# Kernel optimization log

Hardware: AMD Instinct MI355X
Metric: run time of the kernel (lower is better)

Reference implementation:

```python
import jax, jax.numpy as jnp
import numpy as np

B, S, H, NH, L, FF, V, T = 16, 256, 768, 12, 12, 3072, 30522, 9
DH = H // NH
LN_EPS = 1e-12


def _ln(x, g, b):
    m = jnp.mean(x, axis=-1, keepdims=True)
    v = jnp.mean((x - m) ** 2, axis=-1, keepdims=True)
    return (x - m) * jax.lax.rsqrt(v + LN_EPS) * g + b


def setup_inputs():
    key = jax.random.key(0)
    ks = jax.random.split(key, 20)
    n = lambda i, shape: jax.random.normal(ks[i], shape, jnp.float32) * 0.02
    lengths = jax.random.randint(ks[0], (B,), S // 2, S + 1)
    attention_mask = (jnp.arange(S)[None, :] < lengths[:, None]).astype(jnp.int32)
    return {
        "input_ids": jax.random.randint(ks[1], (B, S), 0, V),
        "attention_mask": attention_mask,
        "labels": jax.random.randint(ks[2], (B, S), 0, T),
        "word_emb": n(3, (V, H)),
        "pos_emb": n(4, (512, H)),
        "type_emb": n(5, (2, H)),
        "emb_g": jnp.ones((H,), jnp.float32), "emb_b": jnp.zeros((H,), jnp.float32),
        "lWq": n(6, (L, H, H)), "lbq": jnp.zeros((L, H), jnp.float32),
        "lWk": n(7, (L, H, H)), "lbk": jnp.zeros((L, H), jnp.float32),
        "lWv": n(8, (L, H, H)), "lbv": jnp.zeros((L, H), jnp.float32),
        "lWo": n(9, (L, H, H)), "lbo": jnp.zeros((L, H), jnp.float32),
        "lg1": jnp.ones((L, H), jnp.float32), "lb1": jnp.zeros((L, H), jnp.float32),
        "lWi": n(10, (L, H, FF)), "lbi": jnp.zeros((L, FF), jnp.float32),
        "lWf": n(11, (L, FF, H)), "lbf": jnp.zeros((L, H), jnp.float32),
        "lg2": jnp.ones((L, H), jnp.float32), "lb2": jnp.zeros((L, H), jnp.float32),
        "cls_W": n(12, (H, T)), "cls_b": jnp.zeros((T,), jnp.float32),
        "crf_start": jax.random.uniform(ks[13], (T,), jnp.float32, -0.1, 0.1),
        "crf_end": jax.random.uniform(ks[14], (T,), jnp.float32, -0.1, 0.1),
        "crf_trans": jax.random.uniform(ks[15], (T, T), jnp.float32, -0.1, 0.1),
    }


def _encoder(input_ids, attention_mask, word_emb, pos_emb, type_emb, emb_g, emb_b, layer_stack, cls_W, cls_b):
    x = word_emb[input_ids] + pos_emb[:S][None] + type_emb[0][None, None]  # [B,S,H]
    x = _ln(x, emb_g, emb_b)
    bias = (1.0 - attention_mask.astype(jnp.float32))[:, None, None, :] * -1e9  # [B,1,1,S]
    scale = 1.0 / np.sqrt(DH).astype(np.float32)

    def layer(h, p):
        Wq, bq, Wk, bk, Wv, bv, Wo, bo, g1, b1, Wi, bi, Wf, bf, g2, b2 = p
        q = (h @ Wq + bq).reshape(B, S, NH, DH)
        k = (h @ Wk + bk).reshape(B, S, NH, DH)
        v = (h @ Wv + bv).reshape(B, S, NH, DH)
        att = jax.nn.softmax(jnp.einsum('bqhd,bkhd->bhqk', q, k) * scale + bias, axis=-1)
        ctx = jnp.einsum('bhqk,bkhd->bqhd', att, v).reshape(B, S, H)
        h = _ln(h + ctx @ Wo + bo, g1, b1)
        ff = jax.nn.gelu(h @ Wi + bi, approximate=False) @ Wf + bf
        h = _ln(h + ff, g2, b2)
        return h, None

    x, _ = jax.lax.scan(layer, x, layer_stack)
    return x @ cls_W + cls_b  # [B,S,T]


def _crf_llh(em, tg, m, start, end, trans):
    # pytorch-crf forward, reduction='sum'. em [B,Lc,T], tg [B,Lc] int, m [B,Lc] bool
    mf = m.astype(em.dtype)
    em_sc = jnp.take_along_axis(em, tg[..., None], axis=-1)[..., 0]  # [B,Lc]
    tr_sc = trans[tg[:, :-1], tg[:, 1:]]                             # [B,Lc-1]
    num = start[tg[:, 0]] + em_sc[:, 0] + jnp.sum(mf[:, 1:] * (tr_sc + em_sc[:, 1:]), axis=1)
    seq_ends = jnp.sum(m.astype(jnp.int32), axis=1) - 1
    last_tag = jnp.take_along_axis(tg, seq_ends[:, None], axis=1)[:, 0]
    num = num + end[last_tag]

    def step(score, xs):
        em_t, m_t = xs
        nxt = jax.nn.logsumexp(score[:, :, None] + trans[None] + em_t[:, None, :], axis=1)
        return jnp.where(m_t[:, None], nxt, score), None

    score0 = start[None] + em[:, 0]
    score, _ = jax.lax.scan(step, score0, (em[:, 1:].transpose(1, 0, 2), m[:, 1:].transpose(1, 0)))
    den = jax.nn.logsumexp(score + end[None], axis=1)
    return jnp.sum(num - den)


def _viterbi(em, start, end, trans):
    # decode over the FULL sequence with all-ones mask (matches crf.decode(logits))
    def step(score, em_t):
        cand = score[:, :, None] + trans[None] + em_t[:, None, :]  # [B,T,T]
        return jnp.max(cand, axis=1), jnp.argmax(cand, axis=1)

    score0 = start[None] + em[:, 0]
    score, hist = jax.lax.scan(step, score0, em[:, 1:].transpose(1, 0, 2))  # hist [S-1,B,T]
    last = jnp.argmax(score + end[None], axis=1)  # [B]

    def back(tag, h):
        prev = jnp.take_along_axis(h, tag[:, None], axis=1)[:, 0]
        return prev, prev

    _, rev = jax.lax.scan(back, last, hist, reverse=True)  # rev[i] = tag at time i, i in [0,S-2]
    tags = jnp.concatenate([rev.transpose(1, 0), last[:, None]], axis=1)  # [B,S]
    return tags.astype(jnp.float32)


def reference(input_ids, attention_mask, labels, word_emb, pos_emb, type_emb, emb_g, emb_b,
              lWq, lbq, lWk, lbk, lWv, lbv, lWo, lbo, lg1, lb1, lWi, lbi, lWf, lbf, lg2, lb2,
              cls_W, cls_b, crf_start, crf_end, crf_trans):
    layer_stack = (lWq, lbq, lWk, lbk, lWv, lbv, lWo, lbo, lg1, lb1, lWi, lbi, lWf, lbf, lg2, lb2)
    logits = _encoder(input_ids, attention_mask, word_emb, pos_emb, type_emb, emb_g, emb_b, layer_stack, cls_W, cls_b)
    str_lens = jnp.sum(attention_mask, axis=-1)
    pos = jnp.arange(S)[None, :]
    mask = attention_mask.astype(bool) & (pos > 0) & (pos != (str_lens - 1)[:, None])
    tags_in = jnp.where(mask, labels, jnp.zeros_like(labels))
    loss = -_crf_llh(logits[:, 1:], tags_in[:, 1:], mask[:, 1:], crf_start, crf_end, crf_trans)
    tags = _viterbi(logits, crf_start, crf_end, crf_trans)
    return (loss, tags)
```

## Files before the change

### kernel.cpp

```cpp
#include <hip/hip_runtime.h>

#define B_ 16
#define S_ 256
#define H_ 768
#define NH_ 12
#define DH_ 64
#define L_ 12
#define FF_ 3072
#define T_ 9
#define NTOK (B_*S_)

typedef __attribute__((ext_vector_type(8))) short bfrag;
typedef __attribute__((ext_vector_type(8))) unsigned short us8;
typedef __attribute__((ext_vector_type(4))) float f4;

#define LOG2E_ 1.4426950408889634f
#define LN2_   0.6931471805599453f

__device__ inline unsigned short f2bf(float x) {
    unsigned u = __builtin_bit_cast(unsigned, x);
    return (unsigned short)((u + 0x7fffu + ((u >> 16) & 1u)) >> 16);
}
__device__ inline float bf2f(unsigned short h) {
    unsigned u = ((unsigned)h) << 16;
    return __builtin_bit_cast(float, u);
}
__device__ inline void pack8(const float* v, us8& h, us8& l) {
    #pragma unroll
    for (int j = 0; j < 8; j++) {
        unsigned short hh = f2bf(v[j]);
        h[j] = hh;
        l[j] = f2bf(v[j] - bf2f(hh));
    }
}

__global__ __launch_bounds__(256) void k_conv_w(
    const float* __restrict__ Wq, const float* __restrict__ Wk,
    const float* __restrict__ Wv, const float* __restrict__ Wo,
    const float* __restrict__ Wi, const float* __restrict__ Wf,
    const float* __restrict__ bq, const float* __restrict__ bk, const float* __restrict__ bv,
    float* __restrict__ qkvbias, unsigned short* __restrict__ Wpk)
{
    int bid = blockIdx.x;
    int tid = threadIdx.x;
    if (bid == 0) {
        for (int i = tid; i < 3 * H_; i += 256)
            qkvbias[i] = (i < H_) ? bq[i] : (i < 2 * H_) ? bk[i - H_] : bv[i - 2 * H_];
    }
    const float* src; int Kd, Nd; size_t doff; int t;
    if (bid < 576)       { int m = bid / 144; src = (m == 0) ? Wq : (m == 1) ? Wk : (m == 2) ? Wv : Wo;
                           Kd = H_; Nd = H_; doff = (size_t)m * 73728; t = bid % 144; }
    else if (bid < 1152) { src = Wi; Kd = H_; Nd = FF_; doff = 294912; t = bid - 576; }
    else                 { src = Wf; Kd = FF_; Nd = H_; doff = 589824; t = bid - 1152; }
    int ntn = Nd / 64;
    int tk = t / ntn, tn = t % ntn;
    int k0 = tk * 64, n0 = tn * 64;
    __shared__ float tile[64][65];
    int r = tid >> 6, c = tid & 63;
    #pragma unroll
    for (int i = 0; i < 16; i++)
        tile[r + i * 4][c] = src[(size_t)(k0 + r + i * 4) * Nd + n0 + c];
    __syncthreads();
    #pragma unroll
    for (int e = 0; e < 2; e++) {
        int item = tid * 2 + e;
        int nl = item >> 3, kb = item & 7;
        float v8[8];
        #pragma unroll
        for (int j = 0; j < 8; j++) v8[j] = tile[kb * 8 + j][nl];
        us8 h, l; pack8(v8, h, l);
        unsigned short* p = Wpk + (doff + (size_t)(n0 + nl) * (Kd / 8) + (k0 / 8 + kb)) * 16;
        *reinterpret_cast<us8*>(p) = h;
        *reinterpret_cast<us8*>(p + 8) = l;
    }
}

__global__ __launch_bounds__(128) void k_embed_ln(
    const int* __restrict__ ids, const float* __restrict__ wemb,
    const float* __restrict__ pemb, const float* __restrict__ temb,
    const float* __restrict__ g, const float* __restrict__ bb,
    float* __restrict__ out, unsigned short* __restrict__ out_pk)
{
    int tok = blockIdx.x;
    int s = tok & (S_ - 1);
    int id = ids[tok];
    int tid = threadIdx.x;
    bool act = tid < 96;
    int idx = tid * 8;
    float v8[8];
    float sum = 0.f;
    if (act) {
        const float4* w4 = reinterpret_cast<const float4*>(wemb + (size_t)id * H_ + idx);
        const float4* p4 = reinterpret_cast<const float4*>(pemb + (size_t)s * H_ + idx);
        const float4* t4 = reinterpret_cast<const float4*>(temb + idx);
        #pragma unroll
        for (int q = 0; q < 2; q++) {
            float4 a = w4[q], b = p4[q], c = t4[q];
            v8[q*4+0] = a.x + b.x + c.x; v8[q*4+1] = a.y + b.y + c.y;
            v8[q*4+2] = a.z + b.z + c.z; v8[q*4+3] = a.w + b.w + c.w;
        }
        #pragma unroll
        for (int j = 0; j < 8; j++) sum += v8[j];
    }
    __shared__ float wsum[2], wvar[2];
    #pragma unroll
    for (int o = 32; o > 0; o >>= 1) sum += __shfl_xor(sum, o);
    if ((tid & 63) == 0) wsum[tid >> 6] = sum;
    __syncthreads();
    float mean = (wsum[0] + wsum[1]) * (1.0f / H_);
    float vs = 0.f;
    if (act) {
        for (int j = 0; j < 8; j++) { float d = v8[j] - mean; vs += d * d; }
    }
    #pragma unroll
    for (int o = 32; o > 0; o >>= 1) vs += __shfl_xor(vs, o);
    if ((tid & 63) == 0) wvar[tid >> 6] = vs;
    __syncthreads();
    float inv = 1.0f / sqrtf((wvar[0] + wvar[1]) * (1.0f / H_) + 1e-12f);
    if (act) {
        float o8[8];
        #pragma unroll
        for (int j = 0; j < 8; j++) o8[j] = (v8[j] - mean) * inv * g[idx + j] + bb[idx + j];
        float4* d4 = reinterpret_cast<float4*>(out + (size_t)tok * H_ + idx);
        d4[0] = make_float4(o8[0], o8[1], o8[2], o8[3]);
        d4[1] = make_float4(o8[4], o8[5], o8[6], o8[7]);
        us8 h, l; pack8(o8, h, l);
        unsigned short* p = out_pk + ((size_t)tok * 96 + tid) * 16;
        *reinterpret_cast<us8*>(p) = h;
        *reinterpret_cast<us8*>(p + 8) = l;
    }
}

__global__ __launch_bounds__(128) void k_res_ln(
    const float* __restrict__ x, const float* __restrict__ res,
    const float* __restrict__ g, const float* __restrict__ bb,
    float* __restrict__ out, unsigned short* __restrict__ out_pk)
{
    int tok = blockIdx.x;
    int tid = threadIdx.x;
    bool act = tid < 96;
    int idx = tid * 8;
    float v8[8];
    float sum = 0.f;
    if (act) {
        const float4* x4 = reinterpret_cast<const float4*>(x + (size_t)tok * H_ + idx);
        const float4* r4 = reinterpret_cast<const float4*>(res + (size_t)tok * H_ + idx);
        #pragma unroll
        for (int q = 0; q < 2; q++) {
            float4 a = x4[q], b = r4[q];
            v8[q*4+0] = a.x + b.x; v8[q*4+1] = a.y + b.y;
            v8[q*4+2] = a.z + b.z; v8[q*4+3] = a.w + b.w;
        }
        #pragma unroll
        for (int j = 0; j < 8; j++) sum += v8[j];
    }
    __shared__ float wsum[2], wvar[2];
    #pragma unroll
    for (int o = 32; o > 0; o >>= 1) sum += __shfl_xor(sum, o);
    if ((tid & 63) == 0) wsum[tid >> 6] = sum;
    __syncthreads();
    float mean = (wsum[0] + wsum[1]) * (1.0f / H_);
    float vs = 0.f;
    if (act) {
        for (int j = 0; j < 8; j++) { float d = v8[j] - mean; vs += d * d; }
    }
    #pragma unroll
    for (int o = 32; o > 0; o >>= 1) vs += __shfl_xor(vs, o);
    if ((tid & 63) == 0) wvar[tid >> 6] = vs;
    __syncthreads();
    float inv = 1.0f / sqrtf((wvar[0] + wvar[1]) * (1.0f / H_) + 1e-12f);
    if (act) {
        float o8[8];
        #pragma unroll
        for (int j = 0; j < 8; j++) o8[j] = (v8[j] - mean) * inv * g[idx + j] + bb[idx + j];
        float4* d4 = reinterpret_cast<float4*>(out + (size_t)tok * H_ + idx);
        d4[0] = make_float4(o8[0], o8[1], o8[2], o8[3]);
        d4[1] = make_float4(o8[4], o8[5], o8[6], o8[7]);
        us8 h, l; pack8(o8, h, l);
        unsigned short* p = out_pk + ((size_t)tok * 96 + tid) * 16;
        *reinterpret_cast<us8*>(p) = h;
        *reinterpret_cast<us8*>(p + 8) = l;
    }
}

__global__ __launch_bounds__(256) void k_gemm_pk(
    const unsigned short* __restrict__ A, const unsigned short* __restrict__ Wp,
    const float* __restrict__ bias,
    float* __restrict__ C0, float* __restrict__ C1, float* __restrict__ C2, int cpb,
    unsigned short* __restrict__ Cpk,
    int M, int N, int K, int act)
{
    __shared__ char smem[32768];
    char* smA = smem;
    char* smB = smem + 16384;

    int nbx = N >> 7;
    int nwg = (M >> 7) * nbx;
    int id = blockIdx.x;
    int cpx = nwg >> 3;
    int swz = (id & 7) * cpx + (id >> 3);
    int by = swz / nbx, bx = swz % nbx;
    int m0 = by << 7, n0 = bx << 7;
    int Kb = K >> 3;
    int nst = Kb >> 2;

    int tid = threadIdx.x;
    int lane = tid & 63, wid = tid >> 6;
    int wm = wid >> 1, wn = wid & 1;
    int fr = lane & 15, fq = lane >> 4;

    f4 acc[4][4];
    #pragma unroll
    for (int i = 0; i < 4; i++)
        #pragma unroll
        for (int j = 0; j < 4; j++) acc[i][j] = (f4){0.f, 0.f, 0.f, 0.f};

    const char* agp[4]; const char* bgp[4];
    int alds[4];
    #pragma unroll
    for (int i = 0; i < 4; i++) {
        int off = i * 4096 + tid * 16;
        int row = off >> 7, col = off & 127;
        agp[i] = (const char*)A + (size_t)(m0 + row) * (Kb * 32) + col;
        bgp[i] = (const char*)Wp + (size_t)(n0 + row) * (Kb * 32) + col;
        alds[i] = row * 128 + (col ^ ((row & 7) << 4));
    }

    int afo[4], bfo[4];
    #pragma unroll
    for (int mi = 0; mi < 4; mi++) {
        int r = wm * 64 + fr + mi * 16;
        afo[mi] = r * 128 + ((fq * 32) ^ ((r & 7) << 4));
        int rb = wn * 64 + fr + mi * 16;
        bfo[mi] = rb * 128 + ((fq * 32) ^ ((rb & 7) << 4));
    }

    us8 ra[4], rb[4];
    #pragma unroll
    for (int i = 0; i < 4; i++) {
        ra[i] = *reinterpret_cast<const us8*>(agp[i]);
        rb[i] = *reinterpret_cast<const us8*>(bgp[i]);
    }

    for (int ks = 0; ks < nst; ks++) {
        #pragma unroll
        for (int i = 0; i < 4; i++) {
            *reinterpret_cast<us8*>(smA + alds[i]) = ra[i];
            *reinterpret_cast<us8*>(smB + alds[i]) = rb[i];
        }
        __syncthreads();
        if (ks + 1 < nst) {
            #pragma unroll
            for (int i = 0; i < 4; i++) {
                ra[i] = *reinterpret_cast<const us8*>(agp[i] + (size_t)(ks + 1) * 128);
                rb[i] = *reinterpret_cast<const us8*>(bgp[i] + (size_t)(ks + 1) * 128);
            }
        }
        bfrag ah[4], al[4], bh[4], bl[4];
        #pragma unroll
        for (int mi = 0; mi < 4; mi++) {
            ah[mi] = *reinterpret_cast<const bfrag*>(smA + afo[mi]);
            al[mi] = *reinterpret_cast<const bfrag*>(smA + (afo[mi] ^ 16));
            bh[mi] = *reinterpret_cast<const bfrag*>(smB + bfo[mi]);
            bl[mi] = *reinterpret_cast<const bfrag*>(smB + (bfo[mi] ^ 16));
        }
        #pragma unroll
        for (int mi = 0; mi < 4; mi++) {
            #pragma unroll
            for (int ni = 0; ni < 4; ni++) {
                acc[mi][ni] = __builtin_amdgcn_mfma_f32_16x16x32_bf16(ah[mi], bh[ni], acc[mi][ni], 0, 0, 0);
                acc[mi][ni] = __builtin_amdgcn_mfma_f32_16x16x32_bf16(ah[mi], bl[ni], acc[mi][ni], 0, 0, 0);
                acc[mi][ni] = __builtin_amdgcn_mfma_f32_16x16x32_bf16(al[mi], bh[ni], acc[mi][ni], 0, 0, 0);
            }
        }
        __syncthreads();
    }

    if (act == 0) {
        #pragma unroll
        for (int mi = 0; mi < 4; mi++) {
            #pragma unroll
            for (int ni = 0; ni < 4; ni++) {
                int col = n0 + wn * 64 + ni * 16 + fr;
                float bv = bias[col];
                int buf = col / cpb;
                float* Cp = (buf == 0) ? C0 : (buf == 1) ? C1 : C2;
                int cc = col - buf * cpb;
                #pragma unroll
                for (int r = 0; r < 4; r++) {
                    int row = m0 + wm * 64 + mi * 16 + fq * 4 + r;
                    Cp[(size_t)row * cpb + cc] = acc[mi][ni][r] + bv;
                }
            }
        }
    } else {
        float* ebuf = (float*)smem;
        int Nb = N >> 3;
        #pragma unroll
        for (int mi = 0; mi < 4; mi++) {
            #pragma unroll
            for (int ni = 0; ni < 4; ni++) {
                int col = n0 + wn * 64 + ni * 16 + fr;
                float bv = bias[col];
                #pragma unroll
                for (int r = 0; r < 4; r++) {
                    float v = acc[mi][ni][r] + bv;
                    v = 0.5f * v * (1.0f + erff(v * 0.70710678118654752f));
                    ebuf[(wid * 16 + fq * 4 + r) * 68 + ni * 16 + fr] = v;
                }
            }
            #pragma unroll
            for (int e = 0; e < 2; e++) {
                int item = lane * 2 + e;
                int row16 = item >> 3, kb = item & 7;
                float v8[8];
                #pragma unroll
                for (int j = 0; j < 8; j++) v8[j] = ebuf[(wid * 16 + row16) * 68 + kb * 8 + j];
                us8 h, l; pack8(v8, h, l);
                int grow = m0 + wm * 64 + mi * 16 + row16;
                int gcb = ((n0 + wn * 64) >> 3) + kb;
                unsigned short* p = Cpk + ((size_t)grow * Nb + gcb) * 16;
                *reinterpret_cast<us8*>(p) = h;
                *reinterpret_cast<us8*>(p + 8) = l;
            }
        }
    }
}

#define SM_KH 0
#define SM_KL 5632
#define SM_VH 11264
#define SM_VL 16384
#define SM_PH 21504
#define SM_PL 26624
__global__ __launch_bounds__(256) void k_attn_fused(
    const float* __restrict__ Q, const float* __restrict__ Kb,
    const float* __restrict__ V, const int* __restrict__ amask,
    unsigned short* __restrict__ ctx_pk)
{
    __shared__ char smem[31744];
    unsigned short* KhS = (unsigned short*)(smem + SM_KH);
    unsigned short* KlS = (unsigned short*)(smem + SM_KL);
    unsigned short* VhS = (unsigned short*)(smem + SM_VH);
    unsigned short* VlS = (unsigned short*)(smem + SM_VL);
    unsigned short* PhS = (unsigned short*)(smem + SM_PH);
    unsigned short* PlS = (unsigned short*)(smem + SM_PL);

    int idx = blockIdx.x;
    int qt = idx & 3;
    int hd = (idx >> 2) % NH_;
    int b = idx / (4 * NH_);
    int tid = threadIdx.x;
    int lane = tid & 63, wid = tid >> 6;
    int fr = lane & 15, fq = lane >> 4;

    int q0 = qt * 64 + wid * 16;

    bfrag qh[2], ql[2];
    {
        const float* qbase = Q + ((size_t)(b * S_ + q0 + fr)) * H_ + hd * DH_;
        #pragma unroll
        for (int ks = 0; ks < 2; ks++) {
            const float4* p = reinterpret_cast<const float4*>(qbase + ks * 32 + fq * 8);
            float4 v0 = p[0], v1 = p[1];
            float vv[8] = {v0.x, v0.y, v0.z, v0.w, v1.x, v1.y, v1.z, v1.w};
            #pragma unroll
            for (int j = 0; j < 8; j++) {
                unsigned short h = f2bf(vv[j]);
                qh[ks][j] = (short)h;
                ql[ks][j] = (short)f2bf(vv[j] - bf2f(h));
            }
        }
    }

    f4 o[4];
    #pragma unroll
    for (int i = 0; i < 4; i++) o[i] = (f4){0.f, 0.f, 0.f, 0.f};
    float m[4], l[4];
    #pragma unroll
    for (int r = 0; r < 4; r++) { m[r] = -3e38f; l[r] = 0.f; }

    int kvrow = tid >> 3;
    int dbase = (tid & 7) * 8;

    for (int t = 0; t < 8; t++) {
        {
            const float* src = Kb + ((size_t)(b * S_ + t * 32 + kvrow)) * H_ + hd * DH_ + dbase;
            float4 a4 = reinterpret_cast<const float4*>(src)[0];
            float4 b4 = reinterpret_cast<const float4*>(src)[1];
            float vv[8] = {a4.x, a4.y, a4.z, a4.w, b4.x, b4.y, b4.z, b4.w};
            us8 h, l2;
            #pragma unroll
            for (int j = 0; j < 8; j++) {
                unsigned short hh = f2bf(vv[j]);
                h[j] = hh; l2[j] = f2bf(vv[j] - bf2f(hh));
            }
            *reinterpret_cast<us8*>(&KhS[kvrow * 88 + dbase]) = h;
            *reinterpret_cast<us8*>(&KlS[kvrow * 88 + dbase]) = l2;
        }
        {
            const float* src = V + ((size_t)(b * S_ + t * 32 + kvrow)) * H_ + hd * DH_ + dbase;
            float4 a4 = reinterpret_cast<const float4*>(src)[0];
            float4 b4 = reinterpret_cast<const float4*>(src)[1];
            float vv[8] = {a4.x, a4.y, a4.z, a4.w, b4.x, b4.y, b4.z, b4.w};
            #pragma unroll
            for (int j = 0; j < 8; j++) {
                unsigned short h = f2bf(vv[j]);
                VhS[(dbase + j) * 40 + kvrow] = h;
                VlS[(dbase + j) * 40 + kvrow] = f2bf(vv[j] - bf2f(h));
            }
        }
        __syncthreads();

        f4 s0 = (f4){0.f,0.f,0.f,0.f}, s1 = (f4){0.f,0.f,0.f,0.f};
        #pragma unroll
        for (int ks = 0; ks < 2; ks++) {
            bfrag kbh0 = *reinterpret_cast<const bfrag*>(&KhS[fr * 88 + ks * 32 + fq * 8]);
            bfrag kbl0 = *reinterpret_cast<const bfrag*>(&KlS[fr * 88 + ks * 32 + fq * 8]);
            bfrag kbh1 = *reinterpret_cast<const bfrag*>(&KhS[(16 + fr) * 88 + ks * 32 + fq * 8]);
            bfrag kbl1 = *reinterpret_cast<const bfrag*>(&KlS[(16 + fr) * 88 + ks * 32 + fq * 8]);
            s0 = __builtin_amdgcn_mfma_f32_16x16x32_bf16(qh[ks], kbh0, s0, 0, 0, 0);
            s0 = __builtin_amdgcn_mfma_f32_16x16x32_bf16(qh[ks], kbl0, s0, 0, 0, 0);
            s0 = __builtin_amdgcn_mfma_f32_16x16x32_bf16(ql[ks], kbh0, s0, 0, 0, 0);
            s1 = __builtin_amdgcn_mfma_f32_16x16x32_bf16(qh[ks], kbh1, s1, 0, 0, 0);
            s1 = __builtin_amdgcn_mfma_f32_16x16x32_bf16(qh[ks], kbl1, s1, 0, 0, 0);
            s1 = __builtin_amdgcn_mfma_f32_16x16x32_bf16(ql[ks], kbh1, s1, 0, 0, 0);
        }

        float cb0 = (amask[b * S_ + t * 32 + fr] == 0) ? -1e9f : 0.f;
        float cb1 = (amask[b * S_ + t * 32 + 16 + fr] == 0) ? -1e9f : 0.f;
        float sc0[4], sc1[4], fct[4], pr0[4], pr1[4];
        #pragma unroll
        for (int r = 0; r < 4; r++) {
            sc0[r] = s0[r] * 0.125f + cb0;
            sc1[r] = s1[r] * 0.125f + cb1;
            float tm = fmaxf(sc0[r], sc1[r]);
            #pragma unroll
            for (int od = 1; od < 16; od <<= 1) tm = fmaxf(tm, __shfl_xor(tm, od));
            float mn = fmaxf(m[r], tm);
            fct[r] = expf(m[r] - mn);
            pr0[r] = expf(sc0[r] - mn);
            pr1[r] = expf(sc1[r] - mn);
            float rs = pr0[r] + pr1[r];
            #pragma unroll
            for (int od = 1; od < 16; od <<= 1) rs += __shfl_xor(rs, od);
            l[r] = l[r] * fct[r] + rs;
            m[r] = mn;
        }
        #pragma unroll
        for (int ci = 0; ci < 4; ci++)
            #pragma unroll
            for (int r = 0; r < 4; r++) o[ci][r] *= fct[r];

        #pragma unroll
        for (int r = 0; r < 4; r++) {
            int row = fq * 4 + r;
            unsigned short h0 = f2bf(pr0[r]);
            PhS[wid * 640 + row * 40 + fr] = h0;
            PlS[wid * 640 + row * 40 + fr] = f2bf(pr0[r] - bf2f(h0));
            unsigned short h1 = f2bf(pr1[r]);
            PhS[wid * 640 + row * 40 + 16 + fr] = h1;
            PlS[wid * 640 + row * 40 + 16 + fr] = f2bf(pr1[r] - bf2f(h1));
        }

        bfrag pah = *reinterpret_cast<const bfrag*>(&PhS[wid * 640 + fr * 40 + fq * 8]);
        bfrag pal = *reinterpret_cast<const bfrag*>(&PlS[wid * 640 + fr * 40 + fq * 8]);
        #pragma unroll
        for (int ci = 0; ci < 4; ci++) {
            bfrag vbh = *reinterpret_cast<const bfrag*>(&VhS[(ci * 16 + fr) * 40 + fq * 8]);
            bfrag vbl = *reinterpret_cast<const bfrag*>(&VlS[(ci * 16 + fr) * 40 + fq * 8]);
            o[ci] = __builtin_amdgcn_mfma_f32_16x16x32_bf16(pah, vbh, o[ci], 0, 0, 0);
            o[ci] = __builtin_amdgcn_mfma_f32_16x16x32_bf16(pah, vbl, o[ci], 0, 0, 0);
            o[ci] = __builtin_amdgcn_mfma_f32_16x16x32_bf16(pal, vbh, o[ci], 0, 0, 0);
        }
        __syncthreads();
    }

    __syncthreads();
    float* eb = (float*)smem + wid * 1088;
    #pragma unroll
    for (int r = 0; r < 4; r++) {
        float inv = 1.0f / l[r];
        #pragma unroll
        for (int ci = 0; ci < 4; ci++)
            eb[(fq * 4 + r) * 68 + ci * 16 + fr] = o[ci][r] * inv;
    }
    __syncthreads();
    #pragma unroll
    for (int e = 0; e < 2; e++) {
        int item = lane * 2 + e;
        int row16 = item >> 3, kb = item & 7;
        float v8[8];
        #pragma unroll
        for (int j = 0; j < 8; j++) v8[j] = eb[row16 * 68 + kb * 8 + j];
        us8 h, l2; pack8(v8, h, l2);
        int grow = b * S_ + q0 + row16;
        int gcb = hd * 8 + kb;
        unsigned short* p = ctx_pk + ((size_t)grow * 96 + gcb) * 16;
        *reinterpret_cast<us8*>(p) = h;
        *reinterpret_cast<us8*>(p + 8) = l2;
    }
}

__global__ __launch_bounds__(64) void k_classifier(
    const float* __restrict__ Hs, const float* __restrict__ Wc,
    const float* __restrict__ bc, float* __restrict__ logits)
{
    int tok = blockIdx.x;
    int lane = threadIdx.x;
    const float* hr = Hs + (size_t)tok * H_;
    float acc[T_];
    #pragma unroll
    for (int j = 0; j < T_; j++) acc[j] = 0.f;
    for (int k = lane; k < H_; k += 64) {
        float hv = hr[k];
        const float* wr = Wc + (size_t)k * T_;
        #pragma unroll
        for (int j = 0; j < T_; j++) acc[j] = fmaf(hv, wr[j], acc[j]);
    }
    #pragma unroll
    for (int j = 0; j < T_; j++) {
        float v = acc[j];
        for (int o = 32; o > 0; o >>= 1) v += __shfl_down(v, o);
        if (lane == 0) logits[(size_t)tok * T_ + j] = v + bc[j];
    }
}

__global__ __launch_bounds__(256) void k_crf_vit(
    const float* __restrict__ logits, const int* __restrict__ amask,
    const int* __restrict__ labels, const float* __restrict__ start,
    const float* __restrict__ endv, const float* __restrict__ trans,
    float* __restrict__ out)
{
    int blk = blockIdx.x;
    int tid = threadIdx.x;
    if (blk == 0) {
        __shared__ float res[B_];
        int lane = tid & 63;
        int bb = (tid >> 6) * 4 + (lane >> 4);
        int sj = lane & 15;
        int lb = lane & 48;

        int cnt = 0;
        for (int s = sj; s < S_; s += 16) cnt += amask[bb * S_ + s];
        #pragma unroll
        for (int o = 8; o > 0; o >>= 1) cnt += __shfl_xor(cnt, o);
        int len = cnt;
        int lim = len - 1;

        float num = 0.f;
        for (int s = 2 + sj; s < S_; s += 16) {
            if (s < lim) {
                int tp = labels[bb * S_ + s - 1];
                int tc = labels[bb * S_ + s];
                num += trans[tp * T_ + tc] + logits[((size_t)(bb * S_ + s)) * T_ + tc];
            }
        }
        #pragma unroll
        for (int o = 8; o > 0; o >>= 1) num += __shfl_xor(num, o);
        int tg1 = labels[bb * S_ + 1];
        num += start[tg1] + logits[((size_t)(bb * S_ + 1)) * T_ + tg1];
        num += endv[labels[bb * S_ + (len - 2)]];

        float tc9[T_];
        #pragma unroll
        for (int i = 0; i < T_; i++) tc9[i] = (sj < T_) ? trans[i * T_ + sj] * LOG2E_ : 0.f;
        float score = (sj < T_) ? (start[sj] + logits[((size_t)(bb * S_ + 1)) * T_ + sj]) * LOG2E_ : 0.f;
        const float* embase = logits + (size_t)bb * S_ * T_ + sj;
        float emb[8];
        #pragma unroll
        for (int c = 0; c < 8; c++) emb[c] = (sj < T_) ? embase[(2 + c) * T_] : 0.f;
        for (int s0 = 2; s0 < S_; s0 += 8) {
            #pragma unroll
            for (int c = 0; c < 8; c++) {
                int s = s0 + c;
                if (s < S_) {
                    float em = emb[c];
                    emb[c] = (sj < T_ && s + 8 < S_) ? embase[(size_t)(s + 8) * T_] : 0.f;
                    float si[T_];
                    #pragma unroll
                    for (int i = 0; i < T_; i++) si[i] = __shfl(score, lb + i);
                    float a9[T_];
                    #pragma unroll
                    for (int i = 0; i < T_; i++) a9[i] = si[i] + tc9[i];
                    float mx = a9[0];
                    #pragma unroll
                    for (int i = 1; i < T_; i++) mx = fmaxf(mx, a9[i]);
                    float sum = 0.f;
                    #pragma unroll
                    for (int i = 0; i < T_; i++) sum += exp2f(a9[i] - mx);
                    float nsc = fmaf(em, LOG2E_, mx + log2f(sum));
                    if (s < lim) score = nsc;
                }
            }
        }
        float se = (sj < T_) ? score + endv[sj] * LOG2E_ : -1e30f;
        float fi[T_];
        #pragma unroll
        for (int i = 0; i < T_; i++) fi[i] = __shfl(se, lb + i);
        if (sj == 0) {
            float mx = -1e30f;
            #pragma unroll
            for (int i = 0; i < T_; i++) mx = fmaxf(mx, fi[i]);
            float sum = 0.f;
            #pragma unroll
            for (int i = 0; i < T_; i++) sum += exp2f(fi[i] - mx);
            res[bb] = (mx + log2f(sum)) * LN2_ - num;
        }
        __syncthreads();
        if (tid == 0) {
            float tot = 0.f;
            #pragma unroll
            for (int i = 0; i < B_; i++) tot += res[i];
            out[0] = tot;
        }
    } else {
        if (tid >= 64) return;
        int b = blk - 1;
        int j = tid;
        float* tags_out = out + 1;
        __shared__ unsigned char hist[S_ - 1][T_];
        float tc9[T_];
        #pragma unroll
        for (int i = 0; i < T_; i++) tc9[i] = (j < T_) ? trans[i * T_ + j] : 0.f;
        float score = (j < T_) ? start[j] + logits[((size_t)(b * S_)) * T_ + j] : -1e30f;
        const float* embase = logits + (size_t)b * S_ * T_ + j;
        float emb[8];
        #pragma unroll
        for (int c = 0; c < 8; c++) emb[c] = (j < T_) ? embase[(1 + c) * T_] : 0.f;
        for (int t0 = 1; t0 < S_; t0 += 8) {
            #pragma unroll
            for (int c = 0; c < 8; c++) {
                int t = t0 + c;
                if (t < S_) {
                    float em = emb[c];
                    emb[c] = (j < T_ && t + 8 < S_) ? embase[(size_t)(t + 8) * T_] : 0.f;
                    float si[T_];
                    #pragma unroll
                    for (int i = 0; i < T_; i++) si[i] = __shfl(score, i);
                    float best = -1e30f; int bi = 0;
                    #pragma unroll
                    for (int i = 0; i < T_; i++) {
                        float cv = si[i] + tc9[i];
                        if (cv > best) { best = cv; bi = i; }
                    }
                    if (j < T_) {
                        hist[t - 1][j] = (unsigned char)bi;
                        score = best + em;
                    }
                }
            }
        }
        float se = (j < T_) ? score + endv[j] : -1e30f;
        float fi[T_];
        #pragma unroll
        for (int i = 0; i < T_; i++) fi[i] = __shfl(se, i);
        if (j == 0) {
            float best = -1e30f; int last = 0;
            #pragma unroll
            for (int i = 0; i < T_; i++) if (fi[i] > best) { best = fi[i]; last = i; }
            tags_out[b * S_ + (S_ - 1)] = (float)last;
            int cur = last;
            for (int t = S_ - 2; t >= 0; t--) {
                cur = hist[t][cur];
                tags_out[b * S_ + t] = (float)cur;
            }
        }
    }
}

extern "C" void kernel_launch(void* const* d_in, const int* in_sizes, int n_in,
                              void* d_out, int out_size, void* d_ws, size_t ws_size,
                              hipStream_t stream)
{
    const int*   input_ids = (const int*)d_in[0];
    const int*   amask     = (const int*)d_in[1];
    const int*   labels    = (const int*)d_in[2];
    const float* word_emb  = (const float*)d_in[3];
    const float* pos_emb   = (const float*)d_in[4];
    const float* type_emb  = (const float*)d_in[5];
    const float* emb_g     = (const float*)d_in[6];
    const float* emb_b     = (const float*)d_in[7];
    const float* lWq = (const float*)d_in[8];
    const float* lbq = (const float*)d_in[9];
    const float* lWk = (const float*)d_in[10];
    const float* lbk = (const float*)d_in[11];
    const float* lWv = (const float*)d_in[12];
    const float* lbv = (const float*)d_in[13];
    const float* lWo = (const float*)d_in[14];
    const float* lbo = (const float*)d_in[15];
    const float* lg1 = (const float*)d_in[16];
    const float* lb1 = (const float*)d_in[17];
    const float* lWi = (const float*)d_in[18];
    const float* lbi = (const float*)d_in[19];
    const float* lWf = (const float*)d_in[20];
    const float* lbf = (const float*)d_in[21];
    const float* lg2 = (const float*)d_in[22];
    const float* lb2 = (const float*)d_in[23];
    const float* cls_W = (const float*)d_in[24];
    const float* cls_b = (const float*)d_in[25];
    const float* crf_start = (const float*)d_in[26];
    const float* crf_end   = (const float*)d_in[27];
    const float* crf_trans = (const float*)d_in[28];

    float* out = (float*)d_out;
    float* ws = (float*)d_ws;

    const size_t NH32 = (size_t)NTOK * H_;
    float* h       = ws;
    float* h_pk_f  = ws + NH32;
    float* q       = ws + 2 * NH32;
    float* kbuf    = ws + 3 * NH32;
    float* v       = ws + 4 * NH32;
    float* ctxpk_f = ws + 5 * NH32;
    float* tmp     = ws + 6 * NH32;
    float* Wpk_f   = ws + 7 * NH32;
    float* qkvbias = Wpk_f + 7077888;
    float* logits  = qkvbias + 3 * H_;

    unsigned short* h_pk   = (unsigned short*)h_pk_f;
    unsigned short* ctx_pk = (unsigned short*)ctxpk_f;
    unsigned short* Wpk    = (unsigned short*)Wpk_f;
    unsigned short* big_pk = (unsigned short*)q;

    k_embed_ln<<<NTOK, 128, 0, stream>>>(input_ids, word_emb, pos_emb, type_emb, emb_g, emb_b, h, h_pk);

    const size_t WOFF_O = 221184, WOFF_I = 294912, WOFF_F = 589824;

    for (int l = 0; l < L_; l++) {
        k_conv_w<<<1728, 256, 0, stream>>>(
            lWq + (size_t)l * H_ * H_, lWk + (size_t)l * H_ * H_,
            lWv + (size_t)l * H_ * H_, lWo + (size_t)l * H_ * H_,
            lWi + (size_t)l * H_ * FF_, lWf + (size_t)l * FF_ * H_,
            lbq + (size_t)l * H_, lbk + (size_t)l * H_, lbv + (size_t)l * H_,
            qkvbias, Wpk);

        k_gemm_pk<<<576, 256, 0, stream>>>(h_pk, Wpk, qkvbias,
            q, kbuf, v, H_, nullptr, NTOK, 3 * H_, H_, 0);

        k_attn_fused<<<B_ * NH_ * 4, 256, 0, stream>>>(q, kbuf, v, amask, ctx_pk);

        k_gemm_pk<<<192, 256, 0, stream>>>(ctx_pk, Wpk + WOFF_O * 16, lbo + (size_t)l * H_,
            tmp, tmp, tmp, H_, nullptr, NTOK, H_, H_, 0);

        k_res_ln<<<NTOK, 128, 0, stream>>>(tmp, h, lg1 + (size_t)l * H_, lb1 + (size_t)l * H_, h, h_pk);

        k_gemm_pk<<<768, 256, 0, stream>>>(h_pk, Wpk + WOFF_I * 16, lbi + (size_t)l * FF_,
            tmp, tmp, tmp, FF_, big_pk, NTOK, FF_, H_, 1);

        k_gemm_pk<<<192, 256, 0, stream>>>(big_pk, Wpk + WOFF_F * 16, lbf + (size_t)l * H_,
            tmp, tmp, tmp, H_, nullptr, NTOK, H_, FF_, 0);

        k_res_ln<<<NTOK, 128, 0, stream>>>(tmp, h, lg2 + (size_t)l * H_, lb2 + (size_t)l * H_, h, h_pk);
    }

    k_classifier<<<NTOK, 64, 0, stream>>>(h, cls_W, cls_b, logits);
    k_crf_vit<<<1 + B_, 256, 0, stream>>>(logits, amask, labels, crf_start, crf_end, crf_trans, out);
}
```

Baseline: 4.034 ms.

## Double-buffer LDS tiles in bf16-split GEMM to remove one barrier per k-step

The GEMM kernel now uses two 32KB shared-memory buffers in alternation. The next tile is written to the idle buffer while the current one is read for MFMA, and global loads are issued two steps ahead. This removes the barrier between the LDS store and the fragment reads in each k-iteration. In exchange the shared-memory footprint doubles to 64KB per block, which may reduce the number of resident workgroups per CU.

Result: no change. 4.000 ms (-0.8%).

```diff
diff --git a/kernel.cpp b/kernel.cpp
--- a/kernel.cpp
+++ b/kernel.cpp
@@ -190,9 +190,7 @@
     unsigned short* __restrict__ Cpk,
     int M, int N, int K, int act)
 {
-    __shared__ char smem[32768];
-    char* smA = smem;
-    char* smB = smem + 16384;
+    __shared__ char smem[65536];
 
     int nbx = N >> 7;
     int nwg = (M >> 7) * nbx;
@@ -241,28 +239,44 @@
         ra[i] = *reinterpret_cast<const us8*>(agp[i]);
         rb[i] = *reinterpret_cast<const us8*>(bgp[i]);
     }
+    #pragma unroll
+    for (int i = 0; i < 4; i++) {
+        *reinterpret_cast<us8*>(smem + alds[i]) = ra[i];
+        *reinterpret_cast<us8*>(smem + 16384 + alds[i]) = rb[i];
+    }
+    if (nst > 1) {
+        #pragma unroll
+        for (int i = 0; i < 4; i++) {
+            ra[i] = *reinterpret_cast<const us8*>(agp[i] + 128);
+            rb[i] = *reinterpret_cast<const us8*>(bgp[i] + 128);
+        }
+    }
+    __syncthreads();
 
     for (int ks = 0; ks < nst; ks++) {
-        #pragma unroll
-        for (int i = 0; i < 4; i++) {
-            *reinterpret_cast<us8*>(smA + alds[i]) = ra[i];
-            *reinterpret_cast<us8*>(smB + alds[i]) = rb[i];
-        }
-        __syncthreads();
+        char* cb = smem + (ks & 1) * 32768;
+        char* nb = smem + ((ks + 1) & 1) * 32768;
         if (ks + 1 < nst) {
             #pragma unroll
             for (int i = 0; i < 4; i++) {
-                ra[i] = *reinterpret_cast<const us8*>(agp[i] + (size_t)(ks + 1) * 128);
-                rb[i] = *reinterpret_cast<const us8*>(bgp[i] + (size_t)(ks + 1) * 128);
+                *reinterpret_cast<us8*>(nb + alds[i]) = ra[i];
+                *reinterpret_cast<us8*>(nb + 16384 + alds[i]) = rb[i];
+            }
+            if (ks + 2 < nst) {
+                #pragma unroll
+                for (int i = 0; i < 4; i++) {
+                    ra[i] = *reinterpret_cast<const us8*>(agp[i] + (size_t)(ks + 2) * 128);
+                    rb[i] = *reinterpret_cast<const us8*>(bgp[i] + (size_t)(ks + 2) * 128);
+                }
             }
         }
         bfrag ah[4], al[4], bh[4], bl[4];
         #pragma unroll
         for (int mi = 0; mi < 4; mi++) {
-            ah[mi] = *reinterpret_cast<const bfrag*>(smA + afo[mi]);
-            al[mi] = *reinterpret_cast<const bfrag*>(smA + (afo[mi] ^ 16));
-            bh[mi] = *reinterpret_cast<const bfrag*>(smB + bfo[mi]);
-            bl[mi] = *reinterpret_cast<const bfrag*>(smB + (bfo[mi] ^ 16));
+            ah[mi] = *reinterpret_cast<const bfrag*>(cb + afo[mi]);
+            al[mi] = *reinterpret_cast<const bfrag*>(cb + (afo[mi] ^ 16));
+            bh[mi] = *reinterpret_cast<const bfrag*>(cb + 16384 + bfo[mi]);
+            bl[mi] = *reinterpret_cast<const bfrag*>(cb + 16384 + (bfo[mi] ^ 16));
         }
         #pragma unroll
         for (int mi = 0; mi < 4; mi++) {
```

## Double-buffer GEMM tiles via direct global-to-LDS loads and narrower N tiles

Applied to the files above, without the earlier changes.

The packed-bf16 GEMM now stages A and B tiles straight from global memory into LDS with global_load_lds, double-buffered so the next K-slice loads while MFMAs run on the current one. This replaces the register round-trip and one of the two barriers per step. The kernel is also templated on N-tile width, and the N=768 GEMMs use 64-wide tiles with twice the workgroups to fill more CUs. The costs are double the LDS footprint, which may limit occupancy, and a full vmcnt(0) wait each step that can still serialize loads.

Result: faster. 3.598 ms (-10.8%).

```diff
diff --git a/kernel.cpp b/kernel.cpp
--- a/kernel.cpp
+++ b/kernel.cpp
@@ -9,6 +9,9 @@
 #define FF_ 3072
 #define T_ 9
 #define NTOK (B_*S_)
+
+#define AS1 __attribute__((address_space(1)))
+#define AS3 __attribute__((address_space(3)))
 
 typedef __attribute__((ext_vector_type(8))) short bfrag;
 typedef __attribute__((ext_vector_type(8))) unsigned short us8;
@@ -183,6 +186,7 @@
     }
 }
 
+template<int WNF>
 __global__ __launch_bounds__(256) void k_gemm_pk(
     const unsigned short* __restrict__ A, const unsigned short* __restrict__ Wp,
     const float* __restrict__ bias,
@@ -190,98 +194,120 @@
     unsigned short* __restrict__ Cpk,
     int M, int N, int K, int act)
 {
-    __shared__ char smem[32768];
-    char* smA = smem;
-    char* smB = smem + 16384;
-
-    int nbx = N >> 7;
+    constexpr int BN = WNF * 32;
+    constexpr int BUFSZ = 16384 + BN * 128;
+    __shared__ char smem[2 * BUFSZ];
+    unsigned smb = (unsigned)(size_t)(void*)smem;
+
+    int nbx = N / BN;
     int nwg = (M >> 7) * nbx;
     int id = blockIdx.x;
     int cpx = nwg >> 3;
     int swz = (id & 7) * cpx + (id >> 3);
     int by = swz / nbx, bx = swz % nbx;
-    int m0 = by << 7, n0 = bx << 7;
+    int m0 = by << 7, n0 = bx * BN;
     int Kb = K >> 3;
     int nst = Kb >> 2;
+    int rowbytes = Kb * 32;
 
     int tid = threadIdx.x;
     int lane = tid & 63, wid = tid >> 6;
     int wm = wid >> 1, wn = wid & 1;
     int fr = lane & 15, fq = lane >> 4;
 
-    f4 acc[4][4];
+    f4 acc[4][WNF];
     #pragma unroll
     for (int i = 0; i < 4; i++)
         #pragma unroll
-        for (int j = 0; j < 4; j++) acc[i][j] = (f4){0.f, 0.f, 0.f, 0.f};
-
-    const char* agp[4]; const char* bgp[4];
-    int alds[4];
+        for (int j = 0; j < WNF; j++) acc[i][j] = (f4){0.f, 0.f, 0.f, 0.f};
+
+    const char* agp[4];
+    const char* bgp[WNF];
     #pragma unroll
     for (int i = 0; i < 4; i++) {
-        int off = i * 4096 + tid * 16;
-        int row = off >> 7, col = off & 127;
-        agp[i] = (const char*)A + (size_t)(m0 + row) * (Kb * 32) + col;
-        bgp[i] = (const char*)Wp + (size_t)(n0 + row) * (Kb * 32) + col;
-        alds[i] = row * 128 + (col ^ ((row & 7) << 4));
-    }
-
-    int afo[4], bfo[4];
+        int d = i * 4096 + tid * 16;
+        int row = d >> 7;
+        int colp = (d & 127) ^ ((row & 7) << 4);
+        agp[i] = (const char*)A + (size_t)(m0 + row) * rowbytes + colp;
+    }
+    #pragma unroll
+    for (int i = 0; i < WNF; i++) {
+        int d = i * 4096 + tid * 16;
+        int row = d >> 7;
+        int colp = (d & 127) ^ ((row & 7) << 4);
+        bgp[i] = (const char*)Wp + (size_t)(n0 + row) * rowbytes + colp;
+    }
+
+    int afo[4], bfo[WNF];
     #pragma unroll
     for (int mi = 0; mi < 4; mi++) {
-        int r = wm * 64 + fr + mi * 16;
+        int r = wm * 64 + mi * 16 + fr;
         afo[mi] = r * 128 + ((fq * 32) ^ ((r & 7) << 4));
-        int rb = wn * 64 + fr + mi * 16;
-        bfo[mi] = rb * 128 + ((fq * 32) ^ ((rb & 7) << 4));
-    }
-
-    us8 ra[4], rb[4];
-    #pragma unroll
-    for (int i = 0; i < 4; i++) {
-        ra[i] = *reinterpret_cast<const us8*>(agp[i]);
-        rb[i] = *reinterpret_cast<const us8*>(bgp[i]);
-    }
+    }
+    #pragma unroll
+    for (int ni = 0; ni < WNF; ni++) {
+        int rb = wn * (WNF * 16) + ni * 16 + fr;
+        bfo[ni] = rb * 128 + ((fq * 32) ^ ((rb & 7) << 4));
+    }
+
+    #pragma unroll
+    for (int i = 0; i < 4; i++)
+        __builtin_amdgcn_global_load_lds((const AS1 void*)(size_t)agp[i],
+            (AS3 void*)(unsigned)(smb + i * 4096 + wid * 1024), 16, 0, 0);
+    #pragma unroll
+    for (int i = 0; i < WNF; i++)
+        __builtin_amdgcn_global_load_lds((const AS1 void*)(size_t)bgp[i],
+            (AS3 void*)(unsigned)(smb + 16384 + i * 4096 + wid * 1024), 16, 0, 0);
+    asm volatile("s_waitcnt vmcnt(0)" ::: "memory");
+    __builtin_amdgcn_s_barrier();
+    __builtin_amdgcn_sched_barrier(0);
 
     for (int ks = 0; ks < nst; ks++) {
-        #pragma unroll
-        for (int i = 0; i < 4; i++) {
-            *reinterpret_cast<us8*>(smA + alds[i]) = ra[i];
-            *reinterpret_cast<us8*>(smB + alds[i]) = rb[i];
-        }
-        __syncthreads();
+        unsigned cb = (unsigned)(ks & 1) * BUFSZ;
+        unsigned nb2 = BUFSZ - cb;
         if (ks + 1 < nst) {
-            #pragma unroll
-            for (int i = 0; i < 4; i++) {
-                ra[i] = *reinterpret_cast<const us8*>(agp[i] + (size_t)(ks + 1) * 128);
-                rb[i] = *reinterpret_cast<const us8*>(bgp[i] + (size_t)(ks + 1) * 128);
-            }
-        }
-        bfrag ah[4], al[4], bh[4], bl[4];
+            size_t ko = (size_t)(ks + 1) * 128;
+            #pragma unroll
+            for (int i = 0; i < 4; i++)
+                __builtin_amdgcn_global_load_lds((const AS1 void*)(size_t)(agp[i] + ko),
+                    (AS3 void*)(unsigned)(smb + nb2 + i * 4096 + wid * 1024), 16, 0, 0);
+            #pragma unroll
+            for (int i = 0; i < WNF; i++)
+                __builtin_amdgcn_global_load_lds((const AS1 void*)(size_t)(bgp[i] + ko),
+                    (AS3 void*)(unsigned)(smb + nb2 + 16384 + i * 4096 + wid * 1024), 16, 0, 0);
+        }
+        const char* cbp = smem + cb;
+        bfrag ah[4], al[4], bh[WNF], bl[WNF];
         #pragma unroll
         for (int mi = 0; mi < 4; mi++) {
-            ah[mi] = *reinterpret_cast<const bfrag*>(smA + afo[mi]);
-            al[mi] = *reinterpret_cast<const bfrag*>(smA + (afo[mi] ^ 16));
-            bh[mi] = *reinterpret_cast<const bfrag*>(smB + bfo[mi]);
-            bl[mi] = *reinterpret_cast<const bfrag*>(smB + (bfo[mi] ^ 16));
+            ah[mi] = *reinterpret_cast<const bfrag*>(cbp + afo[mi]);
+            al[mi] = *reinterpret_cast<const bfrag*>(cbp + (afo[mi] ^ 16));
+        }
+        #pragma unroll
+        for (int ni = 0; ni < WNF; ni++) {
+            bh[ni] = *reinterpret_cast<const bfrag*>(cbp + 16384 + bfo[ni]);
+            bl[ni] = *reinterpret_cast<const bfrag*>(cbp + 16384 + (bfo[ni] ^ 16));
         }
         #pragma unroll
         for (int mi = 0; mi < 4; mi++) {
             #pragma unroll
-            for (int ni = 0; ni < 4; ni++) {
+            for (int ni = 0; ni < WNF; ni++) {
                 acc[mi][ni] = __builtin_amdgcn_mfma_f32_16x16x32_bf16(ah[mi], bh[ni], acc[mi][ni], 0, 0, 0);
                 acc[mi][ni] = __builtin_amdgcn_mfma_f32_16x16x32_bf16(ah[mi], bl[ni], acc[mi][ni], 0, 0, 0);
                 acc[mi][ni] = __builtin_amdgcn_mfma_f32_16x16x32_bf16(al[mi], bh[ni], acc[mi][ni], 0, 0, 0);
             }
         }
-        __syncthreads();
+        asm volatile("s_waitcnt vmcnt(0)" ::: "memory");
+        __builtin_amdgcn_s_barrier();
+        __builtin_amdgcn_sched_barrier(0);
     }
 
     if (act == 0) {
         #pragma unroll
         for (int mi = 0; mi < 4; mi++) {
             #pragma unroll
-            for (int ni = 0; ni < 4; ni++) {
-                int col = n0 + wn * 64 + ni * 16 + fr;
+            for (int ni = 0; ni < WNF; ni++) {
+                int col = n0 + wn * (WNF * 16) + ni * 16 + fr;
                 float bv = bias[col];
                 int buf = col / cpb;
                 float* Cp = (buf == 0) ? C0 : (buf == 1) ? C1 : C2;
@@ -299,8 +325,8 @@
         #pragma unroll
         for (int mi = 0; mi < 4; mi++) {
             #pragma unroll
-            for (int ni = 0; ni < 4; ni++) {
-                int col = n0 + wn * 64 + ni * 16 + fr;
+            for (int ni = 0; ni < WNF; ni++) {
+                int col = n0 + wn * (WNF * 16) + ni * 16 + fr;
                 float bv = bias[col];
                 #pragma unroll
                 for (int r = 0; r < 4; r++) {
@@ -735,20 +761,20 @@
             lbq + (size_t)l * H_, lbk + (size_t)l * H_, lbv + (size_t)l * H_,
             qkvbias, Wpk);
 
-        k_gemm_pk<<<576, 256, 0, stream>>>(h_pk, Wpk, qkvbias,
+        k_gemm_pk<4><<<576, 256, 0, stream>>>(h_pk, Wpk, qkvbias,
             q, kbuf, v, H_, nullptr, NTOK, 3 * H_, H_, 0);
 
         k_attn_fused<<<B_ * NH_ * 4, 256, 0, stream>>>(q, kbuf, v, amask, ctx_pk);
 
-        k_gemm_pk<<<192, 256, 0, stream>>>(ctx_pk, Wpk + WOFF_O * 16, lbo + (size_t)l * H_,
+        k_gemm_pk<2><<<384, 256, 0, stream>>>(ctx_pk, Wpk + WOFF_O * 16, lbo + (size_t)l * H_,
             tmp, tmp, tmp, H_, nullptr, NTOK, H_, H_, 0);
 
         k_res_ln<<<NTOK, 128, 0, stream>>>(tmp, h, lg1 + (size_t)l * H_, lb1 + (size_t)l * H_, h, h_pk);
 
-        k_gemm_pk<<<768, 256, 0, stream>>>(h_pk, Wpk + WOFF_I * 16, lbi + (size_t)l * FF_,
+        k_gemm_pk<4><<<768, 256, 0, stream>>>(h_pk, Wpk + WOFF_I * 16, lbi + (size_t)l * FF_,
             tmp, tmp, tmp, FF_, big_pk, NTOK, FF_, H_, 1);
 
-        k_gemm_pk<<<192, 256, 0, stream>>>(big_pk, Wpk + WOFF_F * 16, lbf + (size_t)l * H_,
+        k_gemm_pk<2><<<384, 256, 0, stream>>>(big_pk, Wpk + WOFF_F * 16, lbf + (size_t)l * H_,
             tmp, tmp, tmp, H_, nullptr, NTOK, H_, FF_, 0);
 
         k_res_ln<<<NTOK, 128, 0, stream>>>(tmp, h, lg2 + (size_t)l * H_, lb2 + (size_t)l * H_, h, h_pk);
```
